# Optimization experiments

Hardware: AMD Instinct MI355X
Metric: run time of the kernel (lower is better)

The kernel has to match this reference:

```python
import jax, jax.numpy as jnp
import numpy as np
import math


def setup_inputs() -> dict:
    key = jax.random.key(0)
    ks = jax.random.split(key, 20)
    B, N, HID, H, D = 32, 32, 256, 8, 32
    A = H * D  # all_head_size == hidden_size
    s = 0.02
    inp = {
        "hidden_states": jax.random.normal(ks[0], (B, N, HID), jnp.float32),
        "structure_matrix": jax.random.normal(ks[1], (B, N, N, HID), jnp.float32),
        "triplet_matrix": jax.random.normal(ks[2], (B, N, N, N, D), jnp.float32),
        "attention_mask": jnp.zeros((B, N, N, N), jnp.float32),
        "Wq": jax.random.normal(ks[3], (HID, A), jnp.float32) * s,
        "bq": jnp.zeros((A,), jnp.float32),
        "Wk": jax.random.normal(ks[4], (3 * HID, A), jnp.float32) * s,
        "bk": jnp.zeros((A,), jnp.float32),
        "Wv": jax.random.normal(ks[5], (HID, A), jnp.float32) * s,
        "bv": jnp.zeros((A,), jnp.float32),
        "Wo": jax.random.normal(ks[6], (HID, HID), jnp.float32) * s,
        "bo": jnp.zeros((HID,), jnp.float32),
        "ln_gamma": jnp.ones((HID,), jnp.float32),
        "ln_beta": jnp.zeros((HID,), jnp.float32),
        "Wtq": jax.random.normal(ks[7], (D, D), jnp.float32) * s,
        "btq": jnp.zeros((D,), jnp.float32),
        "Wtk": jax.random.normal(ks[8], (D, D), jnp.float32) * s,
        "btk": jnp.zeros((D,), jnp.float32),
    }
    return inp


def reference(hidden_states, structure_matrix, triplet_matrix, attention_mask,
              Wq, bq, Wk, bk, Wv, bv, Wo, bo, ln_gamma, ln_beta,
              Wtq, btq, Wtk, btk):
    B, N, HID = hidden_states.shape
    D = Wtq.shape[0]
    A = Wq.shape[1]
    H = A // D

    # query: [B, H, N, D]
    q = (hidden_states @ Wq + bq).reshape(B, N, H, D).transpose(0, 2, 1, 3)
    # key input: concat(row-tiled h, col-tiled h, structure) -> [B, N, N, 3*HID]
    h_row = jnp.broadcast_to(hidden_states[:, :, None, :], (B, N, N, HID))
    h_col = jnp.broadcast_to(hidden_states[:, None, :, :], (B, N, N, HID))
    key_in = jnp.concatenate([h_row, h_col, structure_matrix], axis=-1)
    # key: [B, L, R, H, D]
    k = (key_in @ Wk + bk).reshape(B, N, N, H, D)
    # value: [B, N, H, D]
    v = (hidden_states @ Wv + bv).reshape(B, N, H, D)

    # triplet projections (shared across heads): [B, L, R, N, D]
    tq = triplet_matrix @ Wtq + btq
    tk = triplet_matrix @ Wtk + btk

    scores = (
        jnp.einsum('bhnd,blrhd->bhlrn', q, k)
        + jnp.einsum('bhnd,blrnd->bhlrn', q, tq)
        + jnp.einsum('blrhd,blrnd->bhlrn', k, tk)
    )
    scores = scores / math.sqrt(D) + attention_mask[:, None, :, :, :]
    probs = jax.nn.softmax(scores, axis=-1)

    # context: [B, L, R, H, D] -> [B, L, R, A]
    ctx = jnp.einsum('bhlrn,bnhd->blrhd', probs, v).reshape(B, N, N, A)
    out = ctx @ Wo + bo

    # residual + layernorm over last dim (eps=1e-5)
    x = out + structure_matrix
    mu = jnp.mean(x, axis=-1, keepdims=True)
    var = jnp.mean(jnp.square(x - mu), axis=-1, keepdims=True)
    return (x - mu) / jnp.sqrt(var + 1e-5) * ln_gamma + ln_beta
```

## Files before the change

kernel.cpp:

```cpp
#include <hip/hip_runtime.h>


typedef __attribute__((ext_vector_type(8))) short bs8;
typedef __attribute__((ext_vector_type(16))) float fx16;

union FB { unsigned short u[8]; uint4 q; bs8 v; };

__device__ __forceinline__ float bf2f(unsigned short u) {
  return __uint_as_float(((unsigned int)u) << 16);
}
__device__ __forceinline__ float2 bf2x(unsigned int p) {
  float2 r;
  r.x = __uint_as_float(p << 16);
  r.y = __uint_as_float(p & 0xffff0000u);
  return r;
}
__device__ __forceinline__ unsigned short f2bf(float f) {
  unsigned int x = __float_as_uint(f);
  unsigned int r = x + 0x7fffu + ((x >> 16) & 1u);
  return (unsigned short)(r >> 16);
}


__global__ __launch_bounds__(256) void k_prep(
    const float* __restrict__ Wo, const float* __restrict__ Wk,
    unsigned short* __restrict__ WoT, unsigned short* __restrict__ Wk3T,
    unsigned* __restrict__ maps) {
  __shared__ __align__(16) unsigned short tA[32 * 264];
  __shared__ __align__(16) unsigned short tB[32 * 256];
  const int t = threadIdx.x;
  if (blockIdx.x < 256) {
    WoT[blockIdx.x * 256 + t] = f2bf(Wo[t * 256 + blockIdx.x]);
    return;
  }
  if (blockIdx.x < 512) {
    const int c = blockIdx.x & 255;
    Wk3T[c * 256 + t] = f2bf(Wk[(512 + t) * 256 + c]);
    return;
  }
  {
    const int r = t >> 3, j0 = (t & 7) * 4;
#pragma unroll
    for (int j = 0; j < 4; ++j) {
      tA[r * 264 + j0 + j] = f2bf((float)((r * 29 + (j0 + j) * 37) & 31) - 15.5f);
      tB[r * 256 + j0 + j] = f2bf((float)((r * 31 + (j0 + j) * 23) & 31) - 15.5f);
    }
  }
  __syncthreads();
  if (t >= 64) return;
  const int lane = t, hh = lane >> 5, n_l = lane & 31;

  FB ones, rt32, at32;
#pragma unroll
  for (int e = 0; e < 8; ++e) {
    ones.u[e] = f2bf(1.0f);
    rt32.u[e] = f2bf((float)n_l);
    at32.u[e] = f2bf((float)(hh * 8 + e + 1));
  }

  fx16 Dr, Dc;
#pragma unroll
  for (int g = 0; g < 16; ++g) { Dr[g] = 0.f; Dc[g] = 0.f; }
  Dr = __builtin_amdgcn_mfma_f32_32x32x16_bf16(rt32.v, ones.v, Dr, 0, 0, 0);
  Dc = __builtin_amdgcn_mfma_f32_32x32x16_bf16(ones.v, rt32.v, Dc, 0, 0, 0);
  bool okA = true;
  unsigned rp32[4] = {0u, 0u, 0u, 0u};
#pragma unroll
  for (int g = 0; g < 16; ++g) {
    float v = Dr[g] * (1.f / 16.f);
    int iv = __float2int_rn(v);
    okA = okA && (fabsf(v - (float)iv) < 1e-3f) && (iv >= 0) && (iv < 32);
    rp32[g >> 2] |= ((unsigned)(iv & 31)) << (8 * (g & 3));
  }
  float cv32 = Dc[0] * (1.f / 16.f);
  int ci32 = __float2int_rn(cv32);
  okA = okA && (fabsf(cv32 - (float)ci32) < 1e-3f) && (ci32 >= 0) && (ci32 < 32);
#pragma unroll
  for (int g = 1; g < 16; ++g) okA = okA && (Dc[g] == Dc[0]);

  bool okP = true; int myp32 = hh; unsigned pm = 0;
#pragma unroll
  for (int G = 0; G < 2; ++G) {
    FB bind;
#pragma unroll
    for (int e = 0; e < 8; ++e) bind.u[e] = (hh == G) ? f2bf(1.0f) : 0;
    fx16 D;
#pragma unroll
    for (int g = 0; g < 16; ++g) D[g] = 0.f;
    D = __builtin_amdgcn_mfma_f32_32x32x16_bf16(at32.v, bind.v, D, 0, 0, 0);
    float V = D[0];
    int q = __float2int_rn((V - 36.f) * (1.f / 64.f));
    bool slots = true;
#pragma unroll
    for (int g = 1; g < 16; ++g) slots = slots && (D[g] == V);
    okP = okP && slots && (fabsf(V - (36.f + 64.f * (float)q)) < 0.25f) && (q >= 0) && (q < 2);
    pm |= 1u << (q & 1);
    if (hh == G) myp32 = q & 1;
  }
  okP = okP && (pm == 3u);

  bool okS = okP;
  {
    FB a0, a1, b0, b1;
    a0.q = *(const uint4*)&tA[n_l * 264 + 0  + hh * 8];
    a1.q = *(const uint4*)&tA[n_l * 264 + 16 + hh * 8];
    b0.q = *(const uint4*)&tB[n_l * 256 + 0  + myp32 * 8];
    b1.q = *(const uint4*)&tB[n_l * 256 + 16 + myp32 * 8];
    fx16 D;
#pragma unroll
    for (int g = 0; g < 16; ++g) D[g] = 0.f;
    D = __builtin_amdgcn_mfma_f32_32x32x16_bf16(a0.v, b0.v, D, 0, 0, 0);
    D = __builtin_amdgcn_mfma_f32_32x32x16_bf16(a1.v, b1.v, D, 0, 0, 0);
#pragma unroll
    for (int j = 0; j < 16; ++j) {
      int row = (int)((rp32[j >> 2] >> (8 * (j & 3))) & 31u);
      float ref = 0.f;
      for (int k = 0; k < 32; ++k)
        ref += bf2f(tA[row * 264 + k]) * bf2f(tB[ci32 * 256 + k]);
      okS = okS && (D[j] == ref);
    }
  }

#pragma unroll
  for (int q = 0; q < 4; ++q) maps[128 + lane * 4 + q] = rp32[q];
  maps[384 + lane] = (unsigned)ci32;
  maps[514 + lane] = (unsigned)myp32;
  int f32 = __all((okA && okS) ? 1 : 0);
  if (lane == 0) { maps[449] = (unsigned)f32; maps[448] = 0u; }
}

__global__ __launch_bounds__(256) void k_small(
    const float* __restrict__ hidden, const float* __restrict__ Wq,
    const float* __restrict__ bq, const float* __restrict__ Wk,
    const float* __restrict__ Wv, const float* __restrict__ bv,
    unsigned short* __restrict__ qb, unsigned short* __restrict__ vb,
    unsigned short* __restrict__ krb, unsigned short* __restrict__ kcb)
{
  __shared__ float hs[8][256];
  const int j = threadIdx.x;
  const int row0 = blockIdx.x * 8;
#pragma unroll
  for (int m = 0; m < 8; ++m) hs[m][j] = hidden[(size_t)(row0 + m) * 256 + j];
  __syncthreads();
  float aq[8], a1[8], a2[8], av[8];
#pragma unroll
  for (int m = 0; m < 8; ++m) { aq[m] = 0.f; a1[m] = 0.f; a2[m] = 0.f; av[m] = 0.f; }
  for (int i = 0; i < 256; i += 4) {
    float wq[4], w1[4], w2[4], wv[4];
#pragma unroll
    for (int u = 0; u < 4; ++u) {
      wq[u] = Wq[(i + u) * 256 + j];
      w1[u] = Wk[(i + u) * 256 + j];
      w2[u] = Wk[(256 + i + u) * 256 + j];
      wv[u] = Wv[(i + u) * 256 + j];
    }
#pragma unroll
    for (int u = 0; u < 4; ++u)
#pragma unroll
      for (int m = 0; m < 8; ++m) {
        float s = hs[m][i + u];
        aq[m] = fmaf(s, wq[u], aq[m]);
        a1[m] = fmaf(s, w1[u], a1[m]);
        a2[m] = fmaf(s, w2[u], a2[m]);
        av[m] = fmaf(s, wv[u], av[m]);
      }
  }
  float bqv = bq[j], bvv = bv[j];
#pragma unroll
  for (int m = 0; m < 8; ++m) {
    size_t o = (size_t)(row0 + m) * 256 + j;
    qb[o]  = f2bf(aq[m] + bqv);
    vb[o]  = f2bf(av[m] + bvv);
    krb[o] = f2bf(a1[m]);
    kcb[o] = f2bf(a2[m]);
  }
}

__global__ __launch_bounds__(256) void k_kproj(
    const float* __restrict__ structure, const unsigned short* __restrict__ Wk3T,
    const float* __restrict__ bk, const unsigned short* __restrict__ krb,
    const unsigned short* __restrict__ kcb, unsigned short* __restrict__ Kall,
    const unsigned* __restrict__ maps)
{
  const int t = threadIdx.x, w = t >> 6, lane = t & 63;
  const int bl = blockIdx.x, b = bl >> 5;
  const int rowA = lane & 31, hh = lane >> 5;
  unsigned rp[4]; int cdec, myp;
  if (maps[449] == 1u) {
#pragma unroll
    for (int q = 0; q < 4; ++q) rp[q] = maps[128 + lane * 4 + q];
    cdec = (int)maps[384 + lane];
    myp = (int)maps[514 + lane];
  } else {
    cdec = lane & 31; myp = hh;
#pragma unroll
    for (int q = 0; q < 4; ++q) {
      unsigned v = 0;
#pragma unroll
      for (int j2 = 0; j2 < 4; ++j2)
        v |= ((unsigned)((j2 + 8 * q + 4 * hh) & 255)) << (8 * j2);
      rp[q] = v;
    }
  }
  const int col0 = w * 64 + cdec;
  const float* Ap = structure + (size_t)bl * 8192 + rowA * 256 + hh * 8;
  const unsigned short* Bp0 = Wk3T + (size_t)(w * 64 + (lane & 31)) * 256 + myp * 8;
  const unsigned short* Bp1 = Wk3T + (size_t)(w * 64 + 32 + (lane & 31)) * 256 + myp * 8;
  fx16 acc0, acc1;
#pragma unroll
  for (int j = 0; j < 16; ++j) { acc0[j] = 0.f; acc1[j] = 0.f; }
  float4 pa0 = *(const float4*)(Ap);
  float4 pa1 = *(const float4*)(Ap + 4);
  uint4 pb0 = *(const uint4*)(Bp0);
  uint4 pb1 = *(const uint4*)(Bp1);
  for (int k0 = 0; k0 < 256; k0 += 16) {
    float4 ca0 = pa0, ca1 = pa1;
    uint4 cb0 = pb0, cb1 = pb1;
    if (k0 < 240) {
      pa0 = *(const float4*)(Ap + k0 + 16);
      pa1 = *(const float4*)(Ap + k0 + 20);
      pb0 = *(const uint4*)(Bp0 + k0 + 16);
      pb1 = *(const uint4*)(Bp1 + k0 + 16);
    }
    FB af;
    af.u[0] = f2bf(ca0.x); af.u[1] = f2bf(ca0.y); af.u[2] = f2bf(ca0.z); af.u[3] = f2bf(ca0.w);
    af.u[4] = f2bf(ca1.x); af.u[5] = f2bf(ca1.y); af.u[6] = f2bf(ca1.z); af.u[7] = f2bf(ca1.w);
    FB b0, b1;
    b0.q = cb0; b1.q = cb1;
    acc0 = __builtin_amdgcn_mfma_f32_32x32x16_bf16(af.v, b0.v, acc0, 0, 0, 0);
    acc1 = __builtin_amdgcn_mfma_f32_32x32x16_bf16(af.v, b1.v, acc1, 0, 0, 0);
  }
  float bk0 = bk[col0], bk1 = bk[col0 + 32];
  float kr0 = bf2f(krb[(size_t)bl * 256 + col0]);
  float kr1 = bf2f(krb[(size_t)bl * 256 + col0 + 32]);
#pragma unroll
  for (int reg = 0; reg < 16; ++reg) {
    int r = (int)((rp[reg >> 2] >> (8 * (reg & 3))) & 31u);
    const unsigned short* kcp = kcb + ((size_t)b * 32 + r) * 256;
    size_t o = ((size_t)bl * 32 + r) * 256;
    Kall[o + col0]      = f2bf(acc0[reg] + bk0 + kr0 + bf2f(kcp[col0]));
    Kall[o + col0 + 32] = f2bf(acc1[reg] + bk1 + kr1 + bf2f(kcp[col0 + 32]));
  }
}

__global__ __launch_bounds__(256, 2) void k_attn(
    const unsigned short* __restrict__ qb, const unsigned short* __restrict__ vb,
    const unsigned short* __restrict__ Kall,
    const float* __restrict__ triplet, const float* __restrict__ mask,
    const float* __restrict__ Wtq, const float* __restrict__ btq,
    const float* __restrict__ Wtk, const float* __restrict__ btk,
    const unsigned short* __restrict__ WoT, const float* __restrict__ Wo,
    const float* __restrict__ bo, const float* __restrict__ structure,
    const float* __restrict__ gamma, const float* __restrict__ beta,
    const unsigned* __restrict__ maps, float* __restrict__ out)
{
  __shared__ __align__(16) char smem[78272];
  unsigned short* qs = (unsigned short*)smem;
  unsigned short* vs = (unsigned short*)(smem + 16640);
  float* tqb = (float*)(smem + 33024);
  float* tkb = (float*)(smem + 51456);
  float* Kbb = (float*)(smem + 69888);
  float* pbb = (float*)(smem + 74048);

  const int t = threadIdx.x, w = t >> 6, lane = t & 63;
  const int bl = blockIdx.x, b = bl >> 5;
  const int n_l = lane & 31, hh = lane >> 5;

  const int fok = (maps[449] == 1u) ? 1 : 0;
  unsigned rp[4]; int cdec, myp;
  if (fok) {
#pragma unroll
    for (int q = 0; q < 4; ++q) rp[q] = maps[128 + lane * 4 + q];
    cdec = (int)maps[384 + lane];
    myp = (int)maps[514 + lane];
  } else {
    cdec = n_l; myp = hh;
#pragma unroll
    for (int q = 0; q < 4; ++q) {
      unsigned v = 0;
#pragma unroll
      for (int j2 = 0; j2 < 4; ++j2)
        v |= ((unsigned)((j2 + 8 * q + 4 * hh) & 255)) << (8 * j2);
      rp[q] = v;
    }
  }

  {
    const size_t gbase = (size_t)b * 8192;
#pragma unroll
    for (int c = 0; c < 4; ++c) {
      int f = c * 2048 + t * 8;
      int row = f >> 8, col = f & 255;
      uint4 qv = *(const uint4*)(qb + gbase + f);
      uint2 qlo, qhi;
      qlo.x = qv.x; qlo.y = qv.y; qhi.x = qv.z; qhi.y = qv.w;
      *(uint2*)&qs[row * 260 + col] = qlo;
      *(uint2*)&qs[row * 260 + col + 4] = qhi;
      uint4 vv = *(const uint4*)(vb + gbase + f);
      *(uint4*)&vs[row * 256 + col] = vv;
    }
  }
  FB bqf[2], bkf[2];
#pragma unroll
  for (int s = 0; s < 2; ++s)
#pragma unroll
    for (int e2 = 0; e2 < 8; ++e2) {
      int k = s * 16 + myp * 8 + e2;
      bqf[s].u[e2] = f2bf(Wtq[k * 32 + n_l]);
      bkf[s].u[e2] = f2bf(Wtk[k * 32 + n_l]);
    }
  const float btqc = btq[cdec], btkc = btk[cdec];
  __syncthreads();

  const int j0 = lane * 4, hj = lane >> 3;
  float* tqw = tqb + w * (32 * 36);
  float* tkw = tkb + w * (32 * 36);
  float* Kw = Kbb + w * 260;
  float* pw = pbb + w * (8 * 33);
  unsigned int ctxr[8][2];

  const size_t e0 = (size_t)bl * 32 + w * 8;
  float4 t0, t1, t2, t3; uint2 kvp; float mvp;
  {
    const float* Tp = triplet + e0 * 1024 + n_l * 32 + hh * 8;
    t0 = *(const float4*)(Tp);
    t1 = *(const float4*)(Tp + 4);
    t2 = *(const float4*)(Tp + 16);
    t3 = *(const float4*)(Tp + 20);
    kvp = *(const uint2*)(Kall + e0 * 256 + lane * 4);
    mvp = mask[e0 * 32 + n_l];
  }

  for (int i = 0; i < 8; ++i) {
    const size_t e = e0 + i;
    {
      float2 ka = bf2x(kvp.x), kb2 = bf2x(kvp.y);
      float4 kf; kf.x = ka.x; kf.y = ka.y; kf.z = kb2.x; kf.w = kb2.y;
      *(float4*)&Kw[lane * 4] = kf;
    }
    FB a0f, a1f;
    a0f.u[0] = f2bf(t0.x); a0f.u[1] = f2bf(t0.y); a0f.u[2] = f2bf(t0.z); a0f.u[3] = f2bf(t0.w);
    a0f.u[4] = f2bf(t1.x); a0f.u[5] = f2bf(t1.y); a0f.u[6] = f2bf(t1.z); a0f.u[7] = f2bf(t1.w);
    a1f.u[0] = f2bf(t2.x); a1f.u[1] = f2bf(t2.y); a1f.u[2] = f2bf(t2.z); a1f.u[3] = f2bf(t2.w);
    a1f.u[4] = f2bf(t3.x); a1f.u[5] = f2bf(t3.y); a1f.u[6] = f2bf(t3.z); a1f.u[7] = f2bf(t3.w);
    const float mvc = mvp;

    if (i < 7) {
      const float* Tn = triplet + (e + 1) * 1024 + n_l * 32 + hh * 8;
      t0 = *(const float4*)(Tn);
      t1 = *(const float4*)(Tn + 4);
      t2 = *(const float4*)(Tn + 16);
      t3 = *(const float4*)(Tn + 20);
      kvp = *(const uint2*)(Kall + (e + 1) * 256 + lane * 4);
      mvp = mask[(e + 1) * 32 + n_l];
    }

    fx16 atq, atk;
#pragma unroll
    for (int j = 0; j < 16; ++j) { atq[j] = btqc; atk[j] = btkc; }
    atq = __builtin_amdgcn_mfma_f32_32x32x16_bf16(a0f.v, bqf[0].v, atq, 0, 0, 0);
    atq = __builtin_amdgcn_mfma_f32_32x32x16_bf16(a1f.v, bqf[1].v, atq, 0, 0, 0);
    atk = __builtin_amdgcn_mfma_f32_32x32x16_bf16(a0f.v, bkf[0].v, atk, 0, 0, 0);
    atk = __builtin_amdgcn_mfma_f32_32x32x16_bf16(a1f.v, bkf[1].v, atk, 0, 0, 0);

#pragma unroll
    for (int reg = 0; reg < 16; ++reg) {
      int n = (int)((rp[reg >> 2] >> (8 * (reg & 3))) & 31u);
      tqw[n * 36 + cdec] = atq[reg];
      tkw[n * 36 + cdec] = atk[reg];
    }
    __builtin_amdgcn_wave_barrier();

    float sc[4] = {0.f, 0.f, 0.f, 0.f};
#pragma unroll
    for (int dp = 0; dp < 8; ++dp) {
      float4 tq4 = *(const float4*)&tqw[n_l * 36 + dp * 4];
      float4 tk4 = *(const float4*)&tkw[n_l * 36 + dp * 4];
#pragma unroll
      for (int u = 0; u < 4; ++u) {
        int h = u * 2 + hh;
        uint2 q4 = *(const uint2*)&qs[n_l * 260 + h * 32 + dp * 4];
        float4 k4 = *(const float4*)&Kw[h * 32 + dp * 4];
        float2 qa = bf2x(q4.x), qc = bf2x(q4.y);
        sc[u] = fmaf(qa.x, k4.x + tq4.x, fmaf(k4.x, tk4.x, sc[u]));
        sc[u] = fmaf(qa.y, k4.y + tq4.y, fmaf(k4.y, tk4.y, sc[u]));
        sc[u] = fmaf(qc.x, k4.z + tq4.z, fmaf(k4.z, tk4.z, sc[u]));
        sc[u] = fmaf(qc.y, k4.w + tq4.w, fmaf(k4.w, tk4.w, sc[u]));
      }
    }

#pragma unroll
    for (int u = 0; u < 4; ++u) {
      float s = sc[u] * 0.17677669529663687f + mvc;
      float mx = s;
#pragma unroll
      for (int m = 16; m >= 1; m >>= 1) mx = fmaxf(mx, __shfl_xor(mx, m, 64));
      float p = __expf(s - mx);
      float sum = p;
#pragma unroll
      for (int m = 16; m >= 1; m >>= 1) sum += __shfl_xor(sum, m, 64);
      pw[(u * 2 + hh) * 33 + n_l] = p / sum;
    }
    __builtin_amdgcn_wave_barrier();

    {
      float c0 = 0.f, c1 = 0.f, c2 = 0.f, c3 = 0.f;
      const float* prow = pw + hj * 33;
#pragma unroll 8
      for (int n = 0; n < 32; ++n) {
        float p = prow[n];
        uint2 vv = *(const uint2*)&vs[n * 256 + j0];
        float2 va = bf2x(vv.x), vbv = bf2x(vv.y);
        c0 = fmaf(p, va.x, c0); c1 = fmaf(p, va.y, c1);
        c2 = fmaf(p, vbv.x, c2); c3 = fmaf(p, vbv.y, c3);
      }
      ctxr[i][0] = (unsigned)f2bf(c0) | ((unsigned)f2bf(c1) << 16);
      ctxr[i][1] = (unsigned)f2bf(c2) | ((unsigned)f2bf(c3) << 16);
    }
  }
  __syncthreads();

  unsigned short* cxs = (unsigned short*)(smem + 51456);
#pragma unroll
  for (int i = 0; i < 8; ++i) {
    int r = w * 8 + i;
    uint2 st; st.x = ctxr[i][0]; st.y = ctxr[i][1];
    *(uint2*)&cxs[r * 264 + j0] = st;
  }
  __syncthreads();

  float* xb = (float*)smem;
  if (fok) {
    const int col0 = w * 64 + cdec;
    fx16 acc0, acc1;
#pragma unroll
    for (int j = 0; j < 16; ++j) { acc0[j] = 0.f; acc1[j] = 0.f; }
    for (int k0 = 0; k0 < 256; k0 += 16) {
      FB af; af.q = *(const uint4*)&cxs[n_l * 264 + k0 + hh * 8];
      FB b0; b0.q = *(const uint4*)(WoT + (size_t)(w * 64 + n_l) * 256 + k0 + myp * 8);
      FB b1; b1.q = *(const uint4*)(WoT + (size_t)(w * 64 + 32 + n_l) * 256 + k0 + myp * 8);
      acc0 = __builtin_amdgcn_mfma_f32_32x32x16_bf16(af.v, b0.v, acc0, 0, 0, 0);
      acc1 = __builtin_amdgcn_mfma_f32_32x32x16_bf16(af.v, b1.v, acc1, 0, 0, 0);
    }
    float bo0 = bo[col0], bo1 = bo[col0 + 32];
#pragma unroll
    for (int reg = 0; reg < 16; ++reg) {
      int row = (int)((rp[reg >> 2] >> (8 * (reg & 3))) & 31u);
      const float* sp = structure + ((size_t)bl * 32 + row) * 256;
      xb[row * 260 + col0]      = acc0[reg] + bo0 + sp[col0];
      xb[row * 260 + col0 + 32] = acc1[reg] + bo1 + sp[col0 + 32];
    }
  } else {
    const int rg = t >> 5, cg = t & 31;
    float acc[4][8];
#pragma unroll
    for (int a = 0; a < 4; ++a)
#pragma unroll
      for (int c = 0; c < 8; ++c) acc[a][c] = 0.f;
    const float* wb = Wo + cg * 8;
    for (int i8 = 0; i8 < 256; i8 += 8) {
      float cv[4][8];
#pragma unroll
      for (int a = 0; a < 4; ++a) {
        uint4 c4 = *(const uint4*)&cxs[(rg * 4 + a) * 264 + i8];
        float2 x0 = bf2x(c4.x), x1 = bf2x(c4.y), x2 = bf2x(c4.z), x3 = bf2x(c4.w);
        cv[a][0] = x0.x; cv[a][1] = x0.y; cv[a][2] = x1.x; cv[a][3] = x1.y;
        cv[a][4] = x2.x; cv[a][5] = x2.y; cv[a][6] = x3.x; cv[a][7] = x3.y;
      }
#pragma unroll
      for (int s = 0; s < 8; ++s) {
        float4 w0 = *(const float4*)(wb + (i8 + s) * 256);
        float4 w1 = *(const float4*)(wb + (i8 + s) * 256 + 4);
#pragma unroll
        for (int a = 0; a < 4; ++a) {
          float c = cv[a][s];
          acc[a][0] = fmaf(c, w0.x, acc[a][0]);
          acc[a][1] = fmaf(c, w0.y, acc[a][1]);
          acc[a][2] = fmaf(c, w0.z, acc[a][2]);
          acc[a][3] = fmaf(c, w0.w, acc[a][3]);
          acc[a][4] = fmaf(c, w1.x, acc[a][4]);
          acc[a][5] = fmaf(c, w1.y, acc[a][5]);
          acc[a][6] = fmaf(c, w1.z, acc[a][6]);
          acc[a][7] = fmaf(c, w1.w, acc[a][7]);
        }
      }
    }
    float4 bo0 = *(const float4*)(bo + cg * 8);
    float4 bo1 = *(const float4*)(bo + cg * 8 + 4);
#pragma unroll
    for (int a = 0; a < 4; ++a) {
      int row = rg * 4 + a;
      const float* sp = structure + ((size_t)bl * 32 + row) * 256 + cg * 8;
      float4 s0 = *(const float4*)sp;
      float4 s1 = *(const float4*)(sp + 4);
      float4 o0, o1;
      o0.x = acc[a][0] + bo0.x + s0.x;
      o0.y = acc[a][1] + bo0.y + s0.y;
      o0.z = acc[a][2] + bo0.z + s0.z;
      o0.w = acc[a][3] + bo0.w + s0.w;
      o1.x = acc[a][4] + bo1.x + s1.x;
      o1.y = acc[a][5] + bo1.y + s1.y;
      o1.z = acc[a][6] + bo1.z + s1.z;
      o1.w = acc[a][7] + bo1.w + s1.w;
      *(float4*)&xb[row * 260 + cg * 8]     = o0;
      *(float4*)&xb[row * 260 + cg * 8 + 4] = o1;
    }
  }
  __syncthreads();

#pragma unroll
  for (int rr = 0; rr < 8; ++rr) {
    int r = w * 8 + rr;
    float4 x4 = *(const float4*)&xb[r * 260 + lane * 4];
    float s1 = x4.x + x4.y + x4.z + x4.w;
    float s2 = fmaf(x4.x, x4.x, fmaf(x4.y, x4.y, fmaf(x4.z, x4.z, x4.w * x4.w)));
#pragma unroll
    for (int m = 32; m >= 1; m >>= 1) {
      s1 += __shfl_xor(s1, m, 64);
      s2 += __shfl_xor(s2, m, 64);
    }
    float mu = s1 * (1.f / 256.f);
    float var = s2 * (1.f / 256.f) - mu * mu;
    float rstd = rsqrtf(var + 1e-5f);
    float4 g = *(const float4*)(gamma + lane * 4);
    float4 bt = *(const float4*)(beta + lane * 4);
    float4 o;
    o.x = (x4.x - mu) * rstd * g.x + bt.x;
    o.y = (x4.y - mu) * rstd * g.y + bt.y;
    o.z = (x4.z - mu) * rstd * g.z + bt.z;
    o.w = (x4.w - mu) * rstd * g.w + bt.w;
    *(float4*)&out[((size_t)bl * 32 + r) * 256 + lane * 4] = o;
  }
}

extern "C" void kernel_launch(void* const* d_in, const int* in_sizes, int n_in,
                              void* d_out, int out_size, void* d_ws, size_t ws_size,
                              hipStream_t stream) {
  const float* hidden    = (const float*)d_in[0];
  const float* structure = (const float*)d_in[1];
  const float* triplet   = (const float*)d_in[2];
  const float* mask      = (const float*)d_in[3];
  const float* Wq  = (const float*)d_in[4];
  const float* bq  = (const float*)d_in[5];
  const float* Wk  = (const float*)d_in[6];
  const float* bk  = (const float*)d_in[7];
  const float* Wv  = (const float*)d_in[8];
  const float* bv  = (const float*)d_in[9];
  const float* Wo  = (const float*)d_in[10];
  const float* bo  = (const float*)d_in[11];
  const float* gamma = (const float*)d_in[12];
  const float* beta  = (const float*)d_in[13];
  const float* Wtq = (const float*)d_in[14];
  const float* btq = (const float*)d_in[15];
  const float* Wtk = (const float*)d_in[16];
  const float* btk = (const float*)d_in[17];
  float* out = (float*)d_out;

  unsigned short* qb   = (unsigned short*)d_ws;
  unsigned short* vbp  = qb + 262144;
  unsigned short* krb  = vbp + 262144;
  unsigned short* kcb  = krb + 262144;
  unsigned short* WoT  = kcb + 262144;
  unsigned short* Wk3T = WoT + 65536;
  unsigned short* Kall = Wk3T + 65536;
  unsigned* maps = (unsigned*)(Kall + 8388608);

  hipLaunchKernelGGL(k_prep, dim3(513), dim3(256), 0, stream, Wo, Wk, WoT, Wk3T, maps);
  hipLaunchKernelGGL(k_small, dim3(128), dim3(256), 0, stream,
                     hidden, Wq, bq, Wk, Wv, bv, qb, vbp, krb, kcb);
  hipLaunchKernelGGL(k_kproj, dim3(1024), dim3(256), 0, stream,
                     structure, Wk3T, bk, krb, kcb, Kall, maps);
  hipLaunchKernelGGL(k_attn, dim3(1024), dim3(256), 0, stream,
                     qb, vbp, Kall, triplet, mask, Wtq, btq, Wtk, btk,
                     WoT, Wo, bo, structure, gamma, beta, maps, out);
}
```

Before: 172.3 us.

## Fuse key projection into attention kernel, keep K tile in LDS

```diff
diff --git a/kernel.cpp b/kernel.cpp
--- a/kernel.cpp
+++ b/kernel.cpp
@@ -176,91 +176,25 @@
   }
 }
 
-__global__ __launch_bounds__(256) void k_kproj(
-    const float* __restrict__ structure, const unsigned short* __restrict__ Wk3T,
-    const float* __restrict__ bk, const unsigned short* __restrict__ krb,
-    const unsigned short* __restrict__ kcb, unsigned short* __restrict__ Kall,
-    const unsigned* __restrict__ maps)
-{
-  const int t = threadIdx.x, w = t >> 6, lane = t & 63;
-  const int bl = blockIdx.x, b = bl >> 5;
-  const int rowA = lane & 31, hh = lane >> 5;
-  unsigned rp[4]; int cdec, myp;
-  if (maps[449] == 1u) {
-#pragma unroll
-    for (int q = 0; q < 4; ++q) rp[q] = maps[128 + lane * 4 + q];
-    cdec = (int)maps[384 + lane];
-    myp = (int)maps[514 + lane];
-  } else {
-    cdec = lane & 31; myp = hh;
-#pragma unroll
-    for (int q = 0; q < 4; ++q) {
-      unsigned v = 0;
-#pragma unroll
-      for (int j2 = 0; j2 < 4; ++j2)
-        v |= ((unsigned)((j2 + 8 * q + 4 * hh) & 255)) << (8 * j2);
-      rp[q] = v;
-    }
-  }
-  const int col0 = w * 64 + cdec;
-  const float* Ap = structure + (size_t)bl * 8192 + rowA * 256 + hh * 8;
-  const unsigned short* Bp0 = Wk3T + (size_t)(w * 64 + (lane & 31)) * 256 + myp * 8;
-  const unsigned short* Bp1 = Wk3T + (size_t)(w * 64 + 32 + (lane & 31)) * 256 + myp * 8;
-  fx16 acc0, acc1;
-#pragma unroll
-  for (int j = 0; j < 16; ++j) { acc0[j] = 0.f; acc1[j] = 0.f; }
-  float4 pa0 = *(const float4*)(Ap);
-  float4 pa1 = *(const float4*)(Ap + 4);
-  uint4 pb0 = *(const uint4*)(Bp0);
-  uint4 pb1 = *(const uint4*)(Bp1);
-  for (int k0 = 0; k0 < 256; k0 += 16) {
-    float4 ca0 = pa0, ca1 = pa1;
-    uint4 cb0 = pb0, cb1 = pb1;
-    if (k0 < 240) {
-      pa0 = *(const float4*)(Ap + k0 + 16);
-      pa1 = *(const float4*)(Ap + k0 + 20);
-      pb0 = *(const uint4*)(Bp0 + k0 + 16);
-      pb1 = *(const uint4*)(Bp1 + k0 + 16);
-    }
-    FB af;
-    af.u[0] = f2bf(ca0.x); af.u[1] = f2bf(ca0.y); af.u[2] = f2bf(ca0.z); af.u[3] = f2bf(ca0.w);
-    af.u[4] = f2bf(ca1.x); af.u[5] = f2bf(ca1.y); af.u[6] = f2bf(ca1.z); af.u[7] = f2bf(ca1.w);
-    FB b0, b1;
-    b0.q = cb0; b1.q = cb1;
-    acc0 = __builtin_amdgcn_mfma_f32_32x32x16_bf16(af.v, b0.v, acc0, 0, 0, 0);
-    acc1 = __builtin_amdgcn_mfma_f32_32x32x16_bf16(af.v, b1.v, acc1, 0, 0, 0);
-  }
-  float bk0 = bk[col0], bk1 = bk[col0 + 32];
-  float kr0 = bf2f(krb[(size_t)bl * 256 + col0]);
-  float kr1 = bf2f(krb[(size_t)bl * 256 + col0 + 32]);
-#pragma unroll
-  for (int reg = 0; reg < 16; ++reg) {
-    int r = (int)((rp[reg >> 2] >> (8 * (reg & 3))) & 31u);
-    const unsigned short* kcp = kcb + ((size_t)b * 32 + r) * 256;
-    size_t o = ((size_t)bl * 32 + r) * 256;
-    Kall[o + col0]      = f2bf(acc0[reg] + bk0 + kr0 + bf2f(kcp[col0]));
-    Kall[o + col0 + 32] = f2bf(acc1[reg] + bk1 + kr1 + bf2f(kcp[col0 + 32]));
-  }
-}
-
 __global__ __launch_bounds__(256, 2) void k_attn(
     const unsigned short* __restrict__ qb, const unsigned short* __restrict__ vb,
-    const unsigned short* __restrict__ Kall,
     const float* __restrict__ triplet, const float* __restrict__ mask,
     const float* __restrict__ Wtq, const float* __restrict__ btq,
     const float* __restrict__ Wtk, const float* __restrict__ btk,
+    const unsigned short* __restrict__ Wk3T, const float* __restrict__ bk,
+    const unsigned short* __restrict__ krb, const unsigned short* __restrict__ kcb,
     const unsigned short* __restrict__ WoT, const float* __restrict__ Wo,
     const float* __restrict__ bo, const float* __restrict__ structure,
     const float* __restrict__ gamma, const float* __restrict__ beta,
     const unsigned* __restrict__ maps, float* __restrict__ out)
 {
-  __shared__ __align__(16) char smem[78272];
-  unsigned short* qs = (unsigned short*)smem;
-  unsigned short* vs = (unsigned short*)(smem + 16640);
-  float* tqb = (float*)(smem + 33024);
-  float* tkb = (float*)(smem + 51456);
-  float* Kbb = (float*)(smem + 69888);
-  float* pbb = (float*)(smem + 74048);
+  __shared__ __align__(16) char smem[72576];
+  unsigned short* qs  = (unsigned short*)smem;
+  unsigned short* vs  = (unsigned short*)(smem + 16640);
+  unsigned short* tqh = (unsigned short*)(smem + 33024);
+  unsigned short* tkh = (unsigned short*)(smem + 42240);
+  unsigned short* Klds = (unsigned short*)(smem + 51456);
+  float* pbb = (float*)(smem + 68352);
 
   const int t = threadIdx.x, w = t >> 6, lane = t & 63;
   const int bl = blockIdx.x, b = bl >> 5;
@@ -300,6 +234,49 @@
       *(uint4*)&vs[row * 256 + col] = vv;
     }
   }
+
+  {
+    const int rowA = n_l;
+    const int col0 = w * 64 + cdec;
+    const float* Ap = structure + (size_t)bl * 8192 + rowA * 256 + hh * 8;
+    const unsigned short* Bp0 = Wk3T + (size_t)(w * 64 + n_l) * 256 + myp * 8;
+    const unsigned short* Bp1 = Wk3T + (size_t)(w * 64 + 32 + n_l) * 256 + myp * 8;
+    fx16 acc0, acc1;
+#pragma unroll
+    for (int j = 0; j < 16; ++j) { acc0[j] = 0.f; acc1[j] = 0.f; }
+    float4 pa0 = *(const float4*)(Ap);
+    float4 pa1 = *(const float4*)(Ap + 4);
+    uint4 pb0 = *(const uint4*)(Bp0);
+    uint4 pb1 = *(const uint4*)(Bp1);
+    for (int k0 = 0; k0 < 256; k0 += 16) {
+      float4 ca0 = pa0, ca1 = pa1;
+      uint4 cb0 = pb0, cb1 = pb1;
+      if (k0 < 240) {
+        pa0 = *(const float4*)(Ap + k0 + 16);
+        pa1 = *(const float4*)(Ap + k0 + 20);
+        pb0 = *(const uint4*)(Bp0 + k0 + 16);
+        pb1 = *(const uint4*)(Bp1 + k0 + 16);
+      }
+      FB af;
+      af.u[0] = f2bf(ca0.x); af.u[1] = f2bf(ca0.y); af.u[2] = f2bf(ca0.z); af.u[3] = f2bf(ca0.w);
+      af.u[4] = f2bf(ca1.x); af.u[5] = f2bf(ca1.y); af.u[6] = f2bf(ca1.z); af.u[7] = f2bf(ca1.w);
+      FB b0, b1;
+      b0.q = cb0; b1.q = cb1;
+      acc0 = __builtin_amdgcn_mfma_f32_32x32x16_bf16(af.v, b0.v, acc0, 0, 0, 0);
+      acc1 = __builtin_amdgcn_mfma_f32_32x32x16_bf16(af.v, b1.v, acc1, 0, 0, 0);
+    }
+    float bk0 = bk[col0], bk1 = bk[col0 + 32];
+    float kr0 = bf2f(krb[(size_t)bl * 256 + col0]);
+    float kr1 = bf2f(krb[(size_t)bl * 256 + col0 + 32]);
+#pragma unroll
+    for (int reg = 0; reg < 16; ++reg) {
+      int r = (int)((rp[reg >> 2] >> (8 * (reg & 3))) & 31u);
+      const unsigned short* kcp = kcb + ((size_t)b * 32 + r) * 256;
+      Klds[r * 264 + col0]      = f2bf(acc0[reg] + bk0 + kr0 + bf2f(kcp[col0]));
+      Klds[r * 264 + col0 + 32] = f2bf(acc1[reg] + bk1 + kr1 + bf2f(kcp[col0 + 32]));
+    }
+  }
+
   FB bqf[2], bkf[2];
 #pragma unroll
   for (int s = 0; s < 2; ++s)
@@ -313,31 +290,25 @@
   __syncthreads();
 
   const int j0 = lane * 4, hj = lane >> 3;
-  float* tqw = tqb + w * (32 * 36);
-  float* tkw = tkb + w * (32 * 36);
-  float* Kw = Kbb + w * 260;
+  unsigned short* tqw = tqh + w * (32 * 36);
+  unsigned short* tkw = tkh + w * (32 * 36);
   float* pw = pbb + w * (8 * 33);
   unsigned int ctxr[8][2];
 
   const size_t e0 = (size_t)bl * 32 + w * 8;
-  float4 t0, t1, t2, t3; uint2 kvp; float mvp;
+  float4 t0, t1, t2, t3; float mvp;
   {
     const float* Tp = triplet + e0 * 1024 + n_l * 32 + hh * 8;
     t0 = *(const float4*)(Tp);
     t1 = *(const float4*)(Tp + 4);
     t2 = *(const float4*)(Tp + 16);
     t3 = *(const float4*)(Tp + 20);
-    kvp = *(const uint2*)(Kall + e0 * 256 + lane * 4);
     mvp = mask[e0 * 32 + n_l];
   }
 
   for (int i = 0; i < 8; ++i) {
     const size_t e = e0 + i;
-    {
-      float2 ka = bf2x(kvp.x), kb2 = bf2x(kvp.y);
-      float4 kf; kf.x = ka.x; kf.y = ka.y; kf.z = kb2.x; kf.w = kb2.y;
-      *(float4*)&Kw[lane * 4] = kf;
-    }
+    const int r = w * 8 + i;
     FB a0f, a1f;
     a0f.u[0] = f2bf(t0.x); a0f.u[1] = f2bf(t0.y); a0f.u[2] = f2bf(t0.z); a0f.u[3] = f2bf(t0.w);
     a0f.u[4] = f2bf(t1.x); a0f.u[5] = f2bf(t1.y); a0f.u[6] = f2bf(t1.z); a0f.u[7] = f2bf(t1.w);
@@ -351,7 +322,6 @@
       t1 = *(const float4*)(Tn + 4);
       t2 = *(const float4*)(Tn + 16);
       t3 = *(const float4*)(Tn + 20);
-      kvp = *(const uint2*)(Kall + (e + 1) * 256 + lane * 4);
       mvp = mask[(e + 1) * 32 + n_l];
     }
 
@@ -366,26 +336,29 @@
 #pragma unroll
     for (int reg = 0; reg < 16; ++reg) {
       int n = (int)((rp[reg >> 2] >> (8 * (reg & 3))) & 31u);
-      tqw[n * 36 + cdec] = atq[reg];
-      tkw[n * 36 + cdec] = atk[reg];
+      tqw[n * 36 + cdec] = f2bf(atq[reg]);
+      tkw[n * 36 + cdec] = f2bf(atk[reg]);
     }
     __builtin_amdgcn_wave_barrier();
 
     float sc[4] = {0.f, 0.f, 0.f, 0.f};
 #pragma unroll
     for (int dp = 0; dp < 8; ++dp) {
-      float4 tq4 = *(const float4*)&tqw[n_l * 36 + dp * 4];
-      float4 tk4 = *(const float4*)&tkw[n_l * 36 + dp * 4];
+      uint2 tqp = *(const uint2*)&tqw[n_l * 36 + dp * 4];
+      uint2 tkp = *(const uint2*)&tkw[n_l * 36 + dp * 4];
+      float2 tqa = bf2x(tqp.x), tqc = bf2x(tqp.y);
+      float2 tka = bf2x(tkp.x), tkc = bf2x(tkp.y);
 #pragma unroll
       for (int u = 0; u < 4; ++u) {
         int h = u * 2 + hh;
         uint2 q4 = *(const uint2*)&qs[n_l * 260 + h * 32 + dp * 4];
-        float4 k4 = *(const float4*)&Kw[h * 32 + dp * 4];
+        uint2 k4 = *(const uint2*)&Klds[r * 264 + h * 32 + dp * 4];
         float2 qa = bf2x(q4.x), qc = bf2x(q4.y);
-        sc[u] = fmaf(qa.x, k4.x + tq4.x, fmaf(k4.x, tk4.x, sc[u]));
-        sc[u] = fmaf(qa.y, k4.y + tq4.y, fmaf(k4.y, tk4.y, sc[u]));
-        sc[u] = fmaf(qc.x, k4.z + tq4.z, fmaf(k4.z, tk4.z, sc[u]));
-        sc[u] = fmaf(qc.y, k4.w + tq4.w, fmaf(k4.w, tk4.w, sc[u]));
+        float2 ka = bf2x(k4.x), kc = bf2x(k4.y);
+        sc[u] = fmaf(qa.x, ka.x + tqa.x, fmaf(ka.x, tka.x, sc[u]));
+        sc[u] = fmaf(qa.y, ka.y + tqa.y, fmaf(ka.y, tka.y, sc[u]));
+        sc[u] = fmaf(qc.x, kc.x + tqc.x, fmaf(kc.x, tkc.x, sc[u]));
+        sc[u] = fmaf(qc.y, kc.y + tqc.y, fmaf(kc.y, tkc.y, sc[u]));
       }
     }
 
@@ -562,15 +535,13 @@
   unsigned short* kcb  = krb + 262144;
   unsigned short* WoT  = kcb + 262144;
   unsigned short* Wk3T = WoT + 65536;
-  unsigned short* Kall = Wk3T + 65536;
-  unsigned* maps = (unsigned*)(Kall + 8388608);
+  unsigned* maps = (unsigned*)(Wk3T + 65536);
 
   hipLaunchKernelGGL(k_prep, dim3(513), dim3(256), 0, stream, Wo, Wk, WoT, Wk3T, maps);
   hipLaunchKernelGGL(k_small, dim3(128), dim3(256), 0, stream,
                      hidden, Wq, bq, Wk, Wv, bv, qb, vbp, krb, kcb);
-  hipLaunchKernelGGL(k_kproj, dim3(1024), dim3(256), 0, stream,
-                     structure, Wk3T, bk, krb, kcb, Kall, maps);
   hipLaunchKernelGGL(k_attn, dim3(1024), dim3(256), 0, stream,
-                     qb, vbp, Kall, triplet, mask, Wtq, btq, Wtk, btk,
-                     WoT, Wo, bo, structure, gamma, beta, maps, out);
-}
+                     qb, vbp, triplet, mask, Wtq, btq, Wtk, btk,
+                     Wk3T, bk, krb, kcb, WoT, Wo, bo, structure,
+                     gamma, beta, maps, out);
+}
```

After: 171.0 us. Within noise of the previous version (-0.7%).
